# Performance work log

Measured on AMD Instinct MI355X. Metric: run time of the kernel, lower is better.

## Reference

```python
import jax, jax.numpy as jnp
import numpy as np

PATCH = 16
EPS = 1e-5


def _conv_offsets(x, offset_w, offset_b):
    # offset conv: same kernel/stride/padding as the deform conv
    off = jax.lax.conv_general_dilated(
        x, offset_w, window_strides=(PATCH, PATCH), padding='VALID',
        dimension_numbers=('NCHW', 'OIHW', 'NCHW'))
    return off + offset_b[None, :, None, None]


def _deform_conv(x, offset_w, offset_b, dconv_w):
    B, C, H, W = x.shape
    kh = kw = PATCH
    K = kh * kw
    Ho, Wo = H // PATCH, W // PATCH

    off = _conv_offsets(x, offset_w, offset_b)            # [B, 2K, Ho, Wo]
    # mmcv layout: channels are (dy, dx) pairs per kernel point
    off = off.reshape(B, K, 2, Ho, Wo)
    dy = off[:, :, 0].transpose(0, 2, 3, 1)               # [B, Ho, Wo, K]
    dx = off[:, :, 1].transpose(0, 2, 3, 1)

    ii, jj = jnp.meshgrid(jnp.arange(kh), jnp.arange(kw), indexing='ij')
    ki = ii.reshape(-1).astype(x.dtype)                   # [K]
    kj = jj.reshape(-1).astype(x.dtype)
    base_y = (jnp.arange(Ho, dtype=x.dtype) * PATCH)[:, None] + ki[None, :]  # [Ho, K]
    base_x = (jnp.arange(Wo, dtype=x.dtype) * PATCH)[:, None] + kj[None, :]  # [Wo, K]

    py = base_y[None, :, None, :] + dy                    # [B, Ho, Wo, K]
    px = base_x[None, None, :, :] + dx

    y0 = jnp.floor(py); x0 = jnp.floor(px)
    wy1 = py - y0; wx1 = px - x0
    wy0 = 1.0 - wy1; wx0 = 1.0 - wx1
    y0i = y0.astype(jnp.int32); x0i = x0.astype(jnp.int32)
    y1i = y0i + 1;              x1i = x0i + 1

    xt = x.transpose(0, 2, 3, 1)                          # [B, H, W, C]
    bidx = jnp.arange(B)[:, None, None, None]

    def gather(yi, xi):
        ok = ((yi >= 0) & (yi < H) & (xi >= 0) & (xi < W)).astype(x.dtype)
        v = xt[bidx, jnp.clip(yi, 0, H - 1), jnp.clip(xi, 0, W - 1)]  # [B,Ho,Wo,K,C]
        return v * ok[..., None]

    sampled = (gather(y0i, x0i) * (wy0 * wx0)[..., None]
               + gather(y0i, x1i) * (wy0 * wx1)[..., None]
               + gather(y1i, x0i) * (wy1 * wx0)[..., None]
               + gather(y1i, x1i) * (wy1 * wx1)[..., None])  # [B,Ho,Wo,K,C]

    Wk = dconv_w.reshape(dconv_w.shape[0], C, K)          # [O, C, K]
    out = jnp.einsum('bhwkc,ock->bohw', sampled, Wk)      # [B, O, Ho, Wo]
    return out


def setup_inputs() -> dict:
    key = jax.random.key(0)
    ks = jax.random.split(key, 3)
    B, C, H, W = 64, 3, 224, 224
    O = 768
    x = jax.random.normal(ks[0], (B, C, H, W), jnp.float32)
    # small offset weights -> offsets of O(1) pixel, exercising bilinear path
    offset_w = jax.random.normal(ks[1], (2 * PATCH * PATCH, C, PATCH, PATCH), jnp.float32) * 0.01
    offset_b = jnp.zeros((2 * PATCH * PATCH,), jnp.float32)
    dconv_w = jax.random.normal(ks[2], (O, C, PATCH, PATCH), jnp.float32) * 0.02
    bn_gamma = jnp.ones((O,), jnp.float32)
    bn_beta = jnp.zeros((O,), jnp.float32)
    return {"x": x, "offset_w": offset_w, "offset_b": offset_b,
            "dconv_w": dconv_w, "bn_gamma": bn_gamma, "bn_beta": bn_beta}


def reference(x, offset_w, offset_b, dconv_w, bn_gamma, bn_beta):
    B = x.shape[0]
    y = _deform_conv(x, offset_w, offset_b, dconv_w)      # [B, O, Ho, Wo]
    # BatchNorm2d (training-mode batch stats, biased var) per torch semantics
    mean = jnp.mean(y, axis=(0, 2, 3), keepdims=True)
    var = jnp.mean((y - mean) ** 2, axis=(0, 2, 3), keepdims=True)
    yn = (y - mean) * jax.lax.rsqrt(var + EPS)
    yn = yn * bn_gamma[None, :, None, None] + bn_beta[None, :, None, None]
    ya = jax.nn.gelu(yn, approximate=False)               # nn.GELU default = exact
    O, Ho, Wo = ya.shape[1], ya.shape[2], ya.shape[3]
    return ya.reshape(B, O, Ho * Wo).transpose(0, 2, 1)   # [B, N, embed_dim]
```

## Files before the change

### kernel.cpp

```cpp
#include <hip/hip_runtime.h>
#include <math.h>

#define PATCH 16
#define BATCH 64
#define CIN 3
#define HH 224
#define WW 224
#define NPATCH (BATCH*14*14)
#define KDIM 768
#define NOFF 512
#define NOUT 768
#define KPTS 256
#define EPSF 1e-5f
#define CHW (CIN*HH*WW)
#define HWX (HH*WW)
#define NRB (NPATCH/128)

using short8 = __attribute__((ext_vector_type(8))) short;
using f32x4  = __attribute__((ext_vector_type(4))) float;

#define GLOAD16(g, l) __builtin_amdgcn_global_load_lds( \
    (const __attribute__((address_space(1))) void*)(g), \
    (__attribute__((address_space(3))) void*)(l), 16, 0, 0)

__device__ __forceinline__ unsigned short f2bf(float f) {
    unsigned int u = __float_as_uint(f);
    u = (u + 0x7fffu + ((u >> 16) & 1u)) >> 16;
    return (unsigned short)u;
}
__device__ __forceinline__ float bf2f(unsigned short h) {
    return __uint_as_float(((unsigned int)h) << 16);
}
__device__ __forceinline__ float gelu_exact(float v) {
    return 0.5f * v * (1.0f + erff(v * 0.70710678118654752440f));
}

__global__ __launch_bounds__(256) void cvt_bf16(
    const float* __restrict__ in, unsigned short* __restrict__ out, int n4)
{
    int i = blockIdx.x * 256 + threadIdx.x;
    if (i >= n4) return;
    float4 v = ((const float4*)in)[i];
    ushort4 o = make_ushort4(f2bf(v.x), f2bf(v.y), f2bf(v.z), f2bf(v.w));
    ((ushort4*)out)[i] = o;
}

__global__ __launch_bounds__(256) void gemm_offsets(
    const unsigned short* __restrict__ xbf, const unsigned short* __restrict__ Bw,
    const float* __restrict__ offb, unsigned short* __restrict__ off)
{
    __shared__ unsigned short lds[3*8192];
    const int t = threadIdx.x;
    const int lane = t & 63;
    const int w = t >> 6, wr = w >> 1, wc = w & 1;

    int bid = blockIdx.x;
    int idx = (bid & 7)*49 + (bid >> 3);
    const int bm = (idx >> 2) * 128, bn = (idx & 3) * 128;

    const int rq = t >> 2;
    const int ksw = (((t & 3) ^ ((t >> 3) & 3)) << 3);

    const unsigned short* aBase0;
    const unsigned short* aBase1;
    {
        int p0 = bm + rq,      b0 = p0/196, r0 = p0%196;
        int p1 = bm + 64 + rq, b1 = p1/196, r1 = p1%196;
        aBase0 = xbf + (size_t)b0*CHW + (size_t)((r0/14)*PATCH)*WW + (size_t)((r0%14)*PATCH);
        aBase1 = xbf + (size_t)b1*CHW + (size_t)((r1/14)*PATCH)*WW + (size_t)((r1%14)*PATCH);
    }
    const unsigned short* bS0 = Bw + (size_t)(bn + rq)*KDIM + ksw;
    const unsigned short* bS1 = Bw + (size_t)(bn + 64 + rq)*KDIM + ksw;

    const int row_a = wr*64 + (lane & 15);
    const int row_b = wc*64 + (lane & 15);
    const int klocs = (((lane >> 4) ^ ((lane >> 1) & 3)) << 3);

#define STG1(slot, k0) do { \
        unsigned short* d = lds + (slot)*8192 + t*8; \
        int e = (k0) + ksw; \
        size_t xo = (size_t)(e >> 8)*HWX + (size_t)((e >> 4) & 15)*WW + (e & 15); \
        GLOAD16(aBase0 + xo, d); \
        GLOAD16(aBase1 + xo, d + 2048); \
        GLOAD16(bS0 + (k0), d + 4096); \
        GLOAD16(bS1 + (k0), d + 6144); \
    } while(0)

    f32x4 acc[4][4] = {};
    STG1(0, 0); STG1(1, 32);
    asm volatile("s_waitcnt vmcnt(4)" ::: "memory");
    __builtin_amdgcn_s_barrier();
#pragma unroll
    for (int it = 0; it < 24; ++it) {
        if (it + 2 < 24) STG1((it+2)%3, (it+2)*32);
        const unsigned short* As_ = lds + (it%3)*8192;
        const unsigned short* Bs_ = As_ + 4096;
        short8 af[4], bv[4];
#pragma unroll
        for (int m = 0; m < 4; ++m) af[m] = *(const short8*)&As_[(row_a + m*16)*32 + klocs];
#pragma unroll
        for (int n = 0; n < 4; ++n) bv[n] = *(const short8*)&Bs_[(row_b + n*16)*32 + klocs];
#pragma unroll
        for (int m = 0; m < 4; ++m)
#pragma unroll
            for (int n = 0; n < 4; ++n)
                acc[m][n] = __builtin_amdgcn_mfma_f32_16x16x32_bf16(af[m], bv[n], acc[m][n], 0, 0, 0);
        if (it < 22) { asm volatile("s_waitcnt vmcnt(4) lgkmcnt(0)" ::: "memory"); __builtin_amdgcn_s_barrier(); }
        else if (it == 22) { asm volatile("s_waitcnt vmcnt(0) lgkmcnt(0)" ::: "memory"); __builtin_amdgcn_s_barrier(); }
    }
#undef STG1

    const int col0 = bn + wc*64 + (lane & 15);
    const int r0 = (lane >> 4) * 4;
#pragma unroll
    for (int m = 0; m < 4; ++m) {
        int grow = bm + wr*64 + m*16 + r0;
#pragma unroll
        for (int n = 0; n < 4; ++n) {
            int gcol = col0 + n*16;
            float bias = offb[gcol];
#pragma unroll
            for (int r = 0; r < 4; ++r)
                off[(size_t)(grow + r)*NOFF + gcol] = f2bf(acc[m][n][r] + bias);
        }
    }
}

__global__ __launch_bounds__(256) void sampler(
    const unsigned short* __restrict__ xbf, const unsigned int* __restrict__ offu,
    unsigned short* __restrict__ A2)
{
    int p = blockIdx.x;
    int k = threadIdx.x;
    int b = p / 196, rem = p % 196;
    int ho = rem / 14, wo = rem % 14;

    unsigned int d2 = offu[(size_t)p*KPTS + k];
    float dy = __uint_as_float((d2 & 0xffffu) << 16);
    float dx = __uint_as_float(d2 & 0xffff0000u);
    float py = (float)(ho*PATCH + (k >> 4)) + dy;
    float px = (float)(wo*PATCH + (k & 15)) + dx;
    float fy = floorf(py), fx = floorf(px);
    float wy1 = py - fy, wx1 = px - fx;
    float wy0 = 1.f - wy1, wx0 = 1.f - wx1;
    int y0 = (int)fy, x0 = (int)fx;
    int y1 = y0 + 1, x1 = x0 + 1;
    bool oky0 = (y0 >= 0) & (y0 < HH);
    bool oky1 = (y1 >= 0) & (y1 < HH);
    bool okx0 = (x0 >= 0) & (x0 < WW);
    bool okx1 = (x1 >= 0) & (x1 < WW);
    int yc0 = min(max(y0, 0), HH-1), yc1 = min(max(y1, 0), HH-1);
    int xc0 = min(max(x0, 0), WW-1), xc1 = min(max(x1, 0), WW-1);
    float w00 = wy0*wx0, w01 = wy0*wx1, w10 = wy1*wx0, w11 = wy1*wx1;

    const unsigned short* xb = xbf + (size_t)b*CHW;
#pragma unroll
    for (int c = 0; c < CIN; ++c) {
        const unsigned short* xc = xb + (size_t)c*HWX;
        float v00 = (oky0 && okx0) ? bf2f(xc[(size_t)yc0*WW + xc0]) : 0.f;
        float v01 = (oky0 && okx1) ? bf2f(xc[(size_t)yc0*WW + xc1]) : 0.f;
        float v10 = (oky1 && okx0) ? bf2f(xc[(size_t)yc1*WW + xc0]) : 0.f;
        float v11 = (oky1 && okx1) ? bf2f(xc[(size_t)yc1*WW + xc1]) : 0.f;
        float v = v00*w00 + v01*w01 + v10*w10 + v11*w11;
        A2[(size_t)p*KDIM + c*KPTS + k] = f2bf(v);
    }
}

__global__ __launch_bounds__(256) void gemm_deform(
    const unsigned short* __restrict__ A, const unsigned short* __restrict__ Bw,
    float* __restrict__ C, float* __restrict__ psum, float* __restrict__ psq)
{
    __shared__ unsigned short lds[3*8192];
    __shared__ float redS[2][128];
    __shared__ float redQ[2][128];
    const int t = threadIdx.x;
    const int lane = t & 63;
    const int w = t >> 6, wr = w >> 1, wc = w & 1;

    int bid = blockIdx.x;
    int xcd = bid & 7, j = bid >> 3;
    int idx = (xcd < 4) ? xcd*74 + j : 296 + (xcd-4)*73 + j;
    const int rblk = idx / 6;
    const int bm = rblk*128, bn = (idx % 6)*128;

    const int rq = t >> 2;
    const int ksw = (((t & 3) ^ ((t >> 3) & 3)) << 3);

    const unsigned short* aS0 = A + (size_t)(bm + rq)*KDIM + ksw;
    const unsigned short* aS1 = A + (size_t)(bm + 64 + rq)*KDIM + ksw;
    const unsigned short* bS0 = Bw + (size_t)(bn + rq)*KDIM + ksw;
    const unsigned short* bS1 = Bw + (size_t)(bn + 64 + rq)*KDIM + ksw;

    const int row_a = wr*64 + (lane & 15);
    const int row_b = wc*64 + (lane & 15);
    const int klocs = (((lane >> 4) ^ ((lane >> 1) & 3)) << 3);

#define STG2(slot, k0) do { \
        unsigned short* d = lds + (slot)*8192 + t*8; \
        GLOAD16(aS0 + (k0), d); \
        GLOAD16(aS1 + (k0), d + 2048); \
        GLOAD16(bS0 + (k0), d + 4096); \
        GLOAD16(bS1 + (k0), d + 6144); \
    } while(0)

    f32x4 acc[4][4] = {};
    STG2(0, 0); STG2(1, 32);
    asm volatile("s_waitcnt vmcnt(4)" ::: "memory");
    __builtin_amdgcn_s_barrier();
#pragma unroll
    for (int it = 0; it < 24; ++it) {
        if (it + 2 < 24) STG2((it+2)%3, (it+2)*32);
        const unsigned short* As_ = lds + (it%3)*8192;
        const unsigned short* Bs_ = As_ + 4096;
        short8 af[4], bv[4];
#pragma unroll
        for (int m = 0; m < 4; ++m) af[m] = *(const short8*)&As_[(row_a + m*16)*32 + klocs];
#pragma unroll
        for (int n = 0; n < 4; ++n) bv[n] = *(const short8*)&Bs_[(row_b + n*16)*32 + klocs];
#pragma unroll
        for (int m = 0; m < 4; ++m)
#pragma unroll
            for (int n = 0; n < 4; ++n)
                acc[m][n] = __builtin_amdgcn_mfma_f32_16x16x32_bf16(af[m], bv[n], acc[m][n], 0, 0, 0);
        if (it < 22) { asm volatile("s_waitcnt vmcnt(4) lgkmcnt(0)" ::: "memory"); __builtin_amdgcn_s_barrier(); }
        else if (it == 22) { asm volatile("s_waitcnt vmcnt(0) lgkmcnt(0)" ::: "memory"); __builtin_amdgcn_s_barrier(); }
    }
#undef STG2

    float s[4] = {}, q[4] = {};
#pragma unroll
    for (int m = 0; m < 4; ++m)
#pragma unroll
        for (int n = 0; n < 4; ++n)
#pragma unroll
            for (int r = 0; r < 4; ++r) {
                float v = acc[m][n][r];
                s[n] += v; q[n] += v*v;
            }
#pragma unroll
    for (int n = 0; n < 4; ++n) {
        s[n] += __shfl_xor(s[n], 16); q[n] += __shfl_xor(q[n], 16);
        s[n] += __shfl_xor(s[n], 32); q[n] += __shfl_xor(q[n], 32);
    }
    if (lane < 16) {
#pragma unroll
        for (int n = 0; n < 4; ++n) {
            redS[wr][wc*64 + n*16 + lane] = s[n];
            redQ[wr][wc*64 + n*16 + lane] = q[n];
        }
    }
    __syncthreads();

    const int col0 = bn + wc*64 + (lane & 15);
    const int r0 = (lane >> 4) * 4;
#pragma unroll
    for (int m = 0; m < 4; ++m) {
        int grow = bm + wr*64 + m*16 + r0;
#pragma unroll
        for (int n = 0; n < 4; ++n) {
            int gcol = col0 + n*16;
#pragma unroll
            for (int r = 0; r < 4; ++r)
                C[(size_t)(grow + r)*NOUT + gcol] = acc[m][n][r];
        }
    }
    if (t < 128) {
        psum[(size_t)rblk*NOUT + bn + t] = redS[0][t] + redS[1][t];
        psq [(size_t)rblk*NOUT + bn + t] = redQ[0][t] + redQ[1][t];
    }
}

__global__ __launch_bounds__(256) void bn_final(
    const float* __restrict__ psum, const float* __restrict__ psq,
    const float* __restrict__ gamma, const float* __restrict__ beta,
    float* __restrict__ scale, float* __restrict__ shift)
{
    int o = blockIdx.x*256 + threadIdx.x;
    float s = 0.f, q = 0.f;
    for (int i = 0; i < NRB; ++i) {
        s += psum[(size_t)i*NOUT + o];
        q += psq [(size_t)i*NOUT + o];
    }
    float mean = s * (1.0f/(float)NPATCH);
    float var  = q * (1.0f/(float)NPATCH) - mean*mean;
    float inv  = 1.0f / sqrtf(var + EPSF);
    float sc   = gamma[o] * inv;
    scale[o] = sc;
    shift[o] = beta[o] - mean*sc;
}

__global__ __launch_bounds__(256) void norm_gelu(
    float* __restrict__ y, const float* __restrict__ scale,
    const float* __restrict__ shift)
{
    __shared__ float ssc[NOUT], ssh[NOUT];
    for (int i = threadIdx.x; i < NOUT; i += 256) { ssc[i] = scale[i]; ssh[i] = shift[i]; }
    __syncthreads();
    const size_t total4 = (size_t)NPATCH * NOUT / 4;
    for (size_t i = (size_t)blockIdx.x*256 + threadIdx.x; i < total4;
         i += (size_t)gridDim.x*256) {
        float4 v = ((float4*)y)[i];
        int og = (int)(i % (NOUT/4));
        float4 sc = ((const float4*)ssc)[og];
        float4 sh = ((const float4*)ssh)[og];
        v.x = gelu_exact(v.x*sc.x + sh.x);
        v.y = gelu_exact(v.y*sc.y + sh.y);
        v.z = gelu_exact(v.z*sc.z + sh.z);
        v.w = gelu_exact(v.w*sc.w + sh.w);
        ((float4*)y)[i] = v;
    }
}

extern "C" void kernel_launch(void* const* d_in, const int* in_sizes, int n_in,
                              void* d_out, int out_size, void* d_ws, size_t ws_size,
                              hipStream_t stream)
{
    const float* x      = (const float*)d_in[0];
    const float* offw   = (const float*)d_in[1];
    const float* offb   = (const float*)d_in[2];
    const float* dconvw = (const float*)d_in[3];
    const float* gamma  = (const float*)d_in[4];
    const float* beta   = (const float*)d_in[5];
    float* out = (float*)d_out;

    const int NX = BATCH*CHW;
    const int NW1 = NOFF*KDIM;
    const int NW2 = NOUT*KDIM;

    unsigned short* xbf   = (unsigned short*)d_ws;
    unsigned short* wbf1  = xbf  + (size_t)NX;
    unsigned short* wbf2  = wbf1 + (size_t)NW1;
    unsigned short* A2    = wbf2 + (size_t)NW2;
    unsigned short* off   = A2   + (size_t)NPATCH*KDIM;
    float* fscratch = (float*)(off + (size_t)NPATCH*NOFF);
    float* psum  = fscratch;
    float* psq   = psum + NRB*NOUT;
    float* scale = psq  + NRB*NOUT;
    float* shift = scale + NOUT;

    cvt_bf16<<<(NX/4 + 255)/256, 256, 0, stream>>>(x, xbf, NX/4);
    cvt_bf16<<<(NW1/4 + 255)/256, 256, 0, stream>>>(offw, wbf1, NW1/4);
    cvt_bf16<<<(NW2/4 + 255)/256, 256, 0, stream>>>(dconvw, wbf2, NW2/4);

    gemm_offsets<<<392, 256, 0, stream>>>(xbf, wbf1, offb, off);
    sampler<<<NPATCH, 256, 0, stream>>>(xbf, (const unsigned int*)off, A2);
    gemm_deform<<<588, 256, 0, stream>>>(A2, wbf2, out, psum, psq);
    bn_final<<<3, 256, 0, stream>>>(psum, psq, gamma, beta, scale, shift);
    norm_gelu<<<2048, 256, 0, stream>>>(out, scale, shift);
}
```

Baseline: 118.0 us.

## Store GEMM output as bf16, merge conversion kernels, raise MFMA wave priority

The deform GEMM now writes its pre-norm output as bf16 into a workspace buffer, and the norm+GELU pass reads that buffer and writes fp32 to the final output. This halves the intermediate write and read traffic in place of the earlier fp32 in-place pass. The three fp32-to-bf16 conversion launches are merged into one grid-stride kernel, and s_setprio brackets the MFMA blocks in both GEMMs. Rounding the pre-activation to bf16 adds some precision loss before normalization.

Measured after the change: 111.5 us. -5.5%, faster.

```diff
diff --git a/kernel.cpp b/kernel.cpp
--- a/kernel.cpp
+++ b/kernel.cpp
@@ -35,14 +35,24 @@
     return 0.5f * v * (1.0f + erff(v * 0.70710678118654752440f));
 }
 
-__global__ __launch_bounds__(256) void cvt_bf16(
-    const float* __restrict__ in, unsigned short* __restrict__ out, int n4)
-{
-    int i = blockIdx.x * 256 + threadIdx.x;
-    if (i >= n4) return;
-    float4 v = ((const float4*)in)[i];
-    ushort4 o = make_ushort4(f2bf(v.x), f2bf(v.y), f2bf(v.z), f2bf(v.w));
-    ((ushort4*)out)[i] = o;
+#define N4X (BATCH*CHW/4)
+#define N4W1 (NOFF*KDIM/4)
+#define N4W2 (NOUT*KDIM/4)
+#define N4ALL (N4X+N4W1+N4W2)
+
+__global__ __launch_bounds__(256) void cvt_all(
+    const float* __restrict__ x, const float* __restrict__ w1,
+    const float* __restrict__ w2, unsigned short* __restrict__ xbf,
+    unsigned short* __restrict__ wbf1, unsigned short* __restrict__ wbf2)
+{
+    for (int i = blockIdx.x*256 + threadIdx.x; i < N4ALL; i += gridDim.x*256) {
+        const float* src; unsigned short* dst; int j;
+        if (i < N4X)            { src = x;  dst = xbf;  j = i; }
+        else if (i < N4X+N4W1)  { src = w1; dst = wbf1; j = i - N4X; }
+        else                    { src = w2; dst = wbf2; j = i - N4X - N4W1; }
+        float4 v = ((const float4*)src)[j];
+        ((ushort4*)dst)[j] = make_ushort4(f2bf(v.x), f2bf(v.y), f2bf(v.z), f2bf(v.w));
+    }
 }
 
 __global__ __launch_bounds__(256) void gemm_offsets(
@@ -100,11 +110,13 @@
         for (int m = 0; m < 4; ++m) af[m] = *(const short8*)&As_[(row_a + m*16)*32 + klocs];
 #pragma unroll
         for (int n = 0; n < 4; ++n) bv[n] = *(const short8*)&Bs_[(row_b + n*16)*32 + klocs];
+        __builtin_amdgcn_s_setprio(1);
 #pragma unroll
         for (int m = 0; m < 4; ++m)
 #pragma unroll
             for (int n = 0; n < 4; ++n)
                 acc[m][n] = __builtin_amdgcn_mfma_f32_16x16x32_bf16(af[m], bv[n], acc[m][n], 0, 0, 0);
+        __builtin_amdgcn_s_setprio(0);
         if (it < 22) { asm volatile("s_waitcnt vmcnt(4) lgkmcnt(0)" ::: "memory"); __builtin_amdgcn_s_barrier(); }
         else if (it == 22) { asm volatile("s_waitcnt vmcnt(0) lgkmcnt(0)" ::: "memory"); __builtin_amdgcn_s_barrier(); }
     }
@@ -168,7 +180,7 @@
 
 __global__ __launch_bounds__(256) void gemm_deform(
     const unsigned short* __restrict__ A, const unsigned short* __restrict__ Bw,
-    float* __restrict__ C, float* __restrict__ psum, float* __restrict__ psq)
+    unsigned short* __restrict__ Cbf, float* __restrict__ psum, float* __restrict__ psq)
 {
     __shared__ unsigned short lds[3*8192];
     __shared__ float redS[2][128];
@@ -217,11 +229,13 @@
         for (int m = 0; m < 4; ++m) af[m] = *(const short8*)&As_[(row_a + m*16)*32 + klocs];
 #pragma unroll
         for (int n = 0; n < 4; ++n) bv[n] = *(const short8*)&Bs_[(row_b + n*16)*32 + klocs];
+        __builtin_amdgcn_s_setprio(1);
 #pragma unroll
         for (int m = 0; m < 4; ++m)
 #pragma unroll
             for (int n = 0; n < 4; ++n)
                 acc[m][n] = __builtin_amdgcn_mfma_f32_16x16x32_bf16(af[m], bv[n], acc[m][n], 0, 0, 0);
+        __builtin_amdgcn_s_setprio(0);
         if (it < 22) { asm volatile("s_waitcnt vmcnt(4) lgkmcnt(0)" ::: "memory"); __builtin_amdgcn_s_barrier(); }
         else if (it == 22) { asm volatile("s_waitcnt vmcnt(0) lgkmcnt(0)" ::: "memory"); __builtin_amdgcn_s_barrier(); }
     }
@@ -261,7 +275,7 @@
             int gcol = col0 + n*16;
 #pragma unroll
             for (int r = 0; r < 4; ++r)
-                C[(size_t)(grow + r)*NOUT + gcol] = acc[m][n][r];
+                Cbf[(size_t)(grow + r)*NOUT + gcol] = f2bf(acc[m][n][r]);
         }
     }
     if (t < 128) {
@@ -290,24 +304,28 @@
 }
 
 __global__ __launch_bounds__(256) void norm_gelu(
-    float* __restrict__ y, const float* __restrict__ scale,
-    const float* __restrict__ shift)
+    const unsigned short* __restrict__ ybf, float* __restrict__ out,
+    const float* __restrict__ scale, const float* __restrict__ shift)
 {
     __shared__ float ssc[NOUT], ssh[NOUT];
     for (int i = threadIdx.x; i < NOUT; i += 256) { ssc[i] = scale[i]; ssh[i] = shift[i]; }
     __syncthreads();
-    const size_t total4 = (size_t)NPATCH * NOUT / 4;
-    for (size_t i = (size_t)blockIdx.x*256 + threadIdx.x; i < total4;
+    const size_t total8 = (size_t)NPATCH * NOUT / 8;
+    for (size_t i = (size_t)blockIdx.x*256 + threadIdx.x; i < total8;
          i += (size_t)gridDim.x*256) {
-        float4 v = ((float4*)y)[i];
-        int og = (int)(i % (NOUT/4));
-        float4 sc = ((const float4*)ssc)[og];
-        float4 sh = ((const float4*)ssh)[og];
-        v.x = gelu_exact(v.x*sc.x + sh.x);
-        v.y = gelu_exact(v.y*sc.y + sh.y);
-        v.z = gelu_exact(v.z*sc.z + sh.z);
-        v.w = gelu_exact(v.w*sc.w + sh.w);
-        ((float4*)y)[i] = v;
+        uint4 v = ((const uint4*)ybf)[i];
+        int og = (int)(i % (NOUT/8)) * 8;
+        float4 o0, o1;
+        o0.x = gelu_exact(__uint_as_float(v.x << 16)        * ssc[og+0] + ssh[og+0]);
+        o0.y = gelu_exact(__uint_as_float(v.x & 0xffff0000u)* ssc[og+1] + ssh[og+1]);
+        o0.z = gelu_exact(__uint_as_float(v.y << 16)        * ssc[og+2] + ssh[og+2]);
+        o0.w = gelu_exact(__uint_as_float(v.y & 0xffff0000u)* ssc[og+3] + ssh[og+3]);
+        o1.x = gelu_exact(__uint_as_float(v.z << 16)        * ssc[og+4] + ssh[og+4]);
+        o1.y = gelu_exact(__uint_as_float(v.z & 0xffff0000u)* ssc[og+5] + ssh[og+5]);
+        o1.z = gelu_exact(__uint_as_float(v.w << 16)        * ssc[og+6] + ssh[og+6]);
+        o1.w = gelu_exact(__uint_as_float(v.w & 0xffff0000u)* ssc[og+7] + ssh[og+7]);
+        ((float4*)out)[2*i]   = o0;
+        ((float4*)out)[2*i+1] = o1;
     }
 }
 
@@ -323,28 +341,26 @@
     const float* beta   = (const float*)d_in[5];
     float* out = (float*)d_out;
 
-    const int NX = BATCH*CHW;
-    const int NW1 = NOFF*KDIM;
-    const int NW2 = NOUT*KDIM;
+    const size_t NX  = (size_t)BATCH*CHW;
+    const size_t NW1 = (size_t)NOFF*KDIM;
+    const size_t NW2 = (size_t)NOUT*KDIM;
 
     unsigned short* xbf   = (unsigned short*)d_ws;
-    unsigned short* wbf1  = xbf  + (size_t)NX;
-    unsigned short* wbf2  = wbf1 + (size_t)NW1;
-    unsigned short* A2    = wbf2 + (size_t)NW2;
+    unsigned short* wbf1  = xbf  + NX;
+    unsigned short* wbf2  = wbf1 + NW1;
+    unsigned short* A2    = wbf2 + NW2;
     unsigned short* off   = A2   + (size_t)NPATCH*KDIM;
-    float* fscratch = (float*)(off + (size_t)NPATCH*NOFF);
+    unsigned short* ybf   = off  + (size_t)NPATCH*NOFF;
+    float* fscratch = (float*)(ybf + (size_t)NPATCH*NOUT);
     float* psum  = fscratch;
     float* psq   = psum + NRB*NOUT;
     float* scale = psq  + NRB*NOUT;
     float* shift = scale + NOUT;
 
-    cvt_bf16<<<(NX/4 + 255)/256, 256, 0, stream>>>(x, xbf, NX/4);
-    cvt_bf16<<<(NW1/4 + 255)/256, 256, 0, stream>>>(offw, wbf1, NW1/4);
-    cvt_bf16<<<(NW2/4 + 255)/256, 256, 0, stream>>>(dconvw, wbf2, NW2/4);
-
+    cvt_all<<<4096, 256, 0, stream>>>(x, offw, dconvw, xbf, wbf1, wbf2);
     gemm_offsets<<<392, 256, 0, stream>>>(xbf, wbf1, offb, off);
     sampler<<<NPATCH, 256, 0, stream>>>(xbf, (const unsigned int*)off, A2);
-    gemm_deform<<<588, 256, 0, stream>>>(A2, wbf2, out, psum, psq);
+    gemm_deform<<<588, 256, 0, stream>>>(A2, wbf2, ybf, psum, psq);
     bn_final<<<3, 256, 0, stream>>>(psum, psq, gamma, beta, scale, shift);
-    norm_gelu<<<2048, 256, 0, stream>>>(out, scale, shift);
-}
+    norm_gelu<<<2048, 256, 0, stream>>>(ybf, out, scale, shift);
+}
```
